# Kernel tuning notes

Hardware: AMD Instinct MI355X
Metric: run time of the kernel (lower is better)

The kernel has to match this reference:

```python
import jax, jax.numpy as jnp
import numpy as np
from jax import lax

LOW_T = 25.0    # int(0.1 * 255)
HIGH_T = 76.0   # int(0.3 * 255)
HYST_ITERS = 64 # cap on hysteresis propagation sweeps
TG22 = 0.4142135623730951  # tan(22.5 deg)
TG67 = 2.414213562373095   # tan(67.5 deg)

SOBEL_X = jnp.array([[-1., 0., 1.], [-2., 0., 2.], [-1., 0., 1.]], dtype=jnp.float32)
SOBEL_Y = jnp.array([[-1., -2., -1.], [0., 0., 0.], [1., 2., 1.]], dtype=jnp.float32)


def _conv3(x, k):
    # x: [B,H,W]; reflect-101 border like cv2.Sobel default
    xp = jnp.pad(x, ((0, 0), (1, 1), (1, 1)), mode='reflect')
    return lax.conv_general_dilated(xp[:, None], k[None, None], (1, 1), 'VALID')[:, 0]


def _dilate3x3(m):
    # 3x3 max-pool (8-connected dilation); m is nonnegative float 0/1
    return lax.reduce_window(m, jnp.float32(0.0), lax.max, (1, 3, 3), (1, 1, 1), 'SAME')


def canny_edge(image, low, high):
    """Batched Canny. image: [B,C,H,W] in [0,1] -> edges [B,1,H,W] in {0,1}."""
    image = lax.stop_gradient(image)  # mirrors .cpu().detach().numpy()
    B, C, H, W = image.shape
    if C == 3:
        gray = 0.299 * image[:, 0] + 0.587 * image[:, 1] + 0.114 * image[:, 2]
    else:
        gray = image[:, 0]
    # (img*255).astype(np.uint8) == floor toward zero for values in [0,1]
    g = jnp.clip(jnp.floor(gray * 255.0), 0.0, 255.0)

    gx = _conv3(g, SOBEL_X)
    gy = _conv3(g, SOBEL_Y)
    mag = jnp.abs(gx) + jnp.abs(gy)  # cv2 default L2gradient=False -> L1 magnitude

    # --- non-maximum suppression (OpenCV-style direction quantization) ---
    mp = jnp.pad(mag, ((0, 0), (1, 1), (1, 1)))

    def sh(dy, dx):
        return mp[:, 1 + dy:1 + dy + H, 1 + dx:1 + dx + W]

    ax, ay = jnp.abs(gx), jnp.abs(gy)
    horiz = ay <= TG22 * ax              # gradient ~horizontal: compare L/R
    vert = ay >= TG67 * ax               # gradient ~vertical: compare U/D
    diag = ~(horiz | vert)
    same_sign = (gx * gy) >= 0
    d1 = diag & same_sign                # 45 deg diagonal

    keep_h = (mag > sh(0, -1)) & (mag >= sh(0, 1))
    keep_v = (mag > sh(-1, 0)) & (mag >= sh(1, 0))
    keep_d1 = (mag > sh(-1, -1)) & (mag >= sh(1, 1))
    keep_d2 = (mag > sh(-1, 1)) & (mag >= sh(1, -1))
    keep = jnp.where(horiz, keep_h,
           jnp.where(vert, keep_v,
           jnp.where(d1, keep_d1, keep_d2)))
    nms = jnp.where(keep, mag, 0.0)

    # --- double threshold + hysteresis (iterative 8-connected propagation) ---
    weak = (nms > low).astype(jnp.float32)
    strong = (nms > high).astype(jnp.float32)

    def cond(state):
        cur, prev, i = state
        return jnp.logical_and(i < HYST_ITERS, jnp.any(cur != prev))

    def body(state):
        cur, prev, i = state
        new = jnp.minimum(_dilate3x3(cur), weak)          # grow strong into weak
        new = jnp.maximum(new, strong)
        return new, cur, i + 1

    edges, _, _ = lax.while_loop(cond, body, (strong, -jnp.ones_like(strong), 0))
    return edges[:, None]  # [B,1,H,W]


def reference(image_A, image_B):
    image_A = jnp.where(image_A.max() > 1, image_A / 2.0, image_A)
    image_B = jnp.where(image_B.max() > 1, image_B / 2.0, image_B)
    edges_A = canny_edge(image_A, LOW_T, HIGH_T)
    edges_B = canny_edge(image_B, LOW_T, HIGH_T)
    diff = edges_A - edges_B
    return jnp.sqrt(jnp.sum(diff * diff))  # Frobenius norm over all elements


def setup_inputs() -> dict:
    key = jax.random.key(0)
    kA, kB = jax.random.split(key)
    image_A = jax.random.uniform(kA, (32, 3, 512, 512), dtype=jnp.float32)
    image_B = jax.random.uniform(kB, (32, 3, 512, 512), dtype=jnp.float32)
    return {"image_A": image_A, "image_B": image_B}
```

## Files before the change

### kernel.cpp

```cpp
#include <hip/hip_runtime.h>
#include <cstdint>

#define IMG_H 512
#define IMG_W 512
#define WPR 8

typedef unsigned long long u64;

__global__ __launch_bounds__(256) void canny_nms_kernel(
    const float* __restrict__ imgA, const float* __restrict__ imgB,
    u64* __restrict__ strong_out, u64* __restrict__ weak_out)
{
    const int img = blockIdx.z;
    const int ty0 = blockIdx.y * 64;
    const int tx0 = blockIdx.x * 64;
    const float* src = (img < 32) ? imgA + (size_t)img * 3 * IMG_H * IMG_W
                                  : imgB + (size_t)(img - 32) * 3 * IMG_H * IMG_W;

    __shared__ float sg[68][68];
    __shared__ float smag[66][66];
    const int tid = threadIdx.x;

    for (int idx = tid; idx < 68 * 68; idx += 256) {
        int ly = idx / 68, lx = idx - ly * 68;
        int iy = ty0 - 2 + ly, ix = tx0 - 2 + lx;
        iy = iy < 0 ? -iy : (iy > IMG_H - 1 ? 2 * (IMG_H - 1) - iy : iy);
        ix = ix < 0 ? -ix : (ix > IMG_W - 1 ? 2 * (IMG_W - 1) - ix : ix);
        size_t p = (size_t)iy * IMG_W + ix;
        float r   = src[p];
        float gch = src[(size_t)IMG_H * IMG_W + p];
        float b   = src[(size_t)2 * IMG_H * IMG_W + p];
        float gray = 0.299f * r + 0.587f * gch + 0.114f * b;
        sg[ly][lx] = fminf(fmaxf(floorf(gray * 255.0f), 0.0f), 255.0f);
    }
    __syncthreads();

    for (int idx = tid; idx < 66 * 66; idx += 256) {
        int ly = idx / 66, lx = idx - ly * 66;
        int iy = ty0 - 1 + ly, ix = tx0 - 1 + lx;
        float m = 0.0f;
        if (iy >= 0 && iy < IMG_H && ix >= 0 && ix < IMG_W) {
            int a = ly + 1, b = lx + 1;
            float tl = sg[a-1][b-1], tc = sg[a-1][b], tr = sg[a-1][b+1];
            float ml = sg[a][b-1],                    mr = sg[a][b+1];
            float bl = sg[a+1][b-1], bc = sg[a+1][b], br = sg[a+1][b+1];
            float gx = (tr + 2.0f*mr + br) - (tl + 2.0f*ml + bl);
            float gy = (bl + 2.0f*bc + br) - (tl + 2.0f*tc + tr);
            m = fabsf(gx) + fabsf(gy);
        }
        smag[ly][lx] = m;
    }
    __syncthreads();

    const int lane = tid & 63;
    const int wv = tid >> 6;
    for (int ry = wv; ry < 64; ry += 4) {
        int a = ry + 2, b = lane + 2;
        float tl = sg[a-1][b-1], tc = sg[a-1][b], tr = sg[a-1][b+1];
        float ml = sg[a][b-1],                    mr = sg[a][b+1];
        float bl = sg[a+1][b-1], bc = sg[a+1][b], br = sg[a+1][b+1];
        float gx = (tr + 2.0f*mr + br) - (tl + 2.0f*ml + bl);
        float gy = (bl + 2.0f*bc + br) - (tl + 2.0f*tc + tr);
        float ax = fabsf(gx), ay = fabsf(gy);
        int my = ry + 1, mx = lane + 1;
        float mag  = smag[my][mx];
        float n_l  = smag[my][mx-1],   n_r  = smag[my][mx+1];
        float n_t  = smag[my-1][mx],   n_b  = smag[my+1][mx];
        float n_tl = smag[my-1][mx-1], n_br = smag[my+1][mx+1];
        float n_tr = smag[my-1][mx+1], n_bl = smag[my+1][mx-1];
        bool horiz = ay <= 0.4142135623730951f * ax;
        bool vert  = ay >= 2.414213562373095f * ax;
        bool d1 = (!(horiz || vert)) && (gx * gy >= 0.0f);
        bool keep_h  = (mag > n_l)  && (mag >= n_r);
        bool keep_v  = (mag > n_t)  && (mag >= n_b);
        bool keep_d1 = (mag > n_tl) && (mag >= n_br);
        bool keep_d2 = (mag > n_tr) && (mag >= n_bl);
        bool keep = horiz ? keep_h : (vert ? keep_v : (d1 ? keep_d1 : keep_d2));
        float nms = keep ? mag : 0.0f;
        u64 wweak   = __ballot(nms > 25.0f);
        u64 wstrong = __ballot(nms > 76.0f);
        if (lane == 0) {
            size_t o = ((size_t)img * IMG_H + (ty0 + ry)) * WPR + blockIdx.x;
            weak_out[o]   = wweak;
            strong_out[o] = wstrong;
        }
    }
}

__global__ __launch_bounds__(256) void hyst_kernel(
    const u64* __restrict__ strong_in, const u64* __restrict__ weak_in,
    u64* __restrict__ edges)
{
    const int img = blockIdx.z;
    const int ty = blockIdx.y, tx = blockIdx.x;
    const int t = threadIdx.x;

    __shared__ u64 sh[4][256];
    __shared__ int sflag;

    const int row0 = ty * 128 - 64;
    const int wc0  = tx * 2 - 1;
    const size_t ibase = (size_t)img * IMG_H * WPR;

    u64 c[4], wk[4];
    {
        int gr = row0 + t;
        bool rok = (gr >= 0 && gr < IMG_H);
        #pragma unroll
        for (int j = 0; j < 4; ++j) {
            int wc = wc0 + j;
            bool ok = rok && wc >= 0 && wc < WPR;
            size_t o = ibase + (size_t)gr * WPR + wc;
            c[j]  = ok ? strong_in[o] : 0ULL;
            wk[j] = ok ? weak_in[o]   : 0ULL;
        }
    }
    if (t == 0) sflag = 0;
    __syncthreads();

    for (int it = 0; it < 64; ++it) {
        u64 h[4];
        h[0] = c[0] | (c[0] << 1) | (c[0] >> 1) | (c[1] << 63);
        h[1] = c[1] | (c[1] << 1) | (c[1] >> 1) | (c[0] >> 63) | (c[2] << 63);
        h[2] = c[2] | (c[2] << 1) | (c[2] >> 1) | (c[1] >> 63) | (c[3] << 63);
        h[3] = c[3] | (c[3] << 1) | (c[3] >> 1) | (c[2] >> 63);
        #pragma unroll
        for (int j = 0; j < 4; ++j) sh[j][t] = h[j];
        __syncthreads();

        u64 n[4] = {h[0], h[1], h[2], h[3]};
        if (t > 0) {
            #pragma unroll
            for (int j = 0; j < 4; ++j) n[j] |= sh[j][t - 1];
        }
        if (t < 255) {
            #pragma unroll
            for (int j = 0; j < 4; ++j) n[j] |= sh[j][t + 1];
        }
        #pragma unroll
        for (int j = 0; j < 4; ++j) n[j] &= wk[j];

        u64 delta = (n[0] ^ c[0]) | (n[1] ^ c[1]) | (n[2] ^ c[2]) | (n[3] ^ c[3]);
        if (delta) sflag = 1;
        __syncthreads();
        int f = sflag;
        __syncthreads();
        if (t == 0) sflag = 0;
        #pragma unroll
        for (int j = 0; j < 4; ++j) c[j] = n[j];
        if (!f) break;
    }

    if (t >= 64 && t < 192) {
        int gr = row0 + t;
        size_t o = ibase + (size_t)gr * WPR;
        edges[o + (wc0 + 1)] = c[1];
        edges[o + (wc0 + 2)] = c[2];
    }
}

__global__ __launch_bounds__(256) void diff_kernel(
    const u64* __restrict__ edges, unsigned int* __restrict__ counter)
{
    size_t i = (size_t)blockIdx.x * 256 + threadIdx.x;
    size_t p = i >> 12;
    size_t k = i & 4095;
    u64 a = edges[p * 4096 + k];
    u64 b = edges[(p + 32) * 4096 + k];
    unsigned int v = (unsigned int)__popcll(a ^ b);
    #pragma unroll
    for (int off = 32; off > 0; off >>= 1) v += __shfl_down(v, off);
    if ((threadIdx.x & 63) == 0) atomicAdd(counter, v);
}

__global__ void finalize_kernel(const unsigned int* __restrict__ counter,
                                float* __restrict__ out)
{
    out[0] = sqrtf((float)(*counter));
}

extern "C" void kernel_launch(void* const* d_in, const int* in_sizes, int n_in,
                              void* d_out, int out_size, void* d_ws, size_t ws_size,
                              hipStream_t stream) {
    const float* imgA = (const float*)d_in[0];
    const float* imgB = (const float*)d_in[1];
    float* out = (float*)d_out;
    char* ws = (char*)d_ws;
    u64* strong_m = (u64*)(ws);
    u64* weak_m   = (u64*)(ws + (2u << 20));
    u64* edges    = (u64*)(ws + (4u << 20));
    unsigned int* counter = (unsigned int*)(ws + (6u << 20));

    hipMemsetAsync(counter, 0, sizeof(unsigned int), stream);

    dim3 g1(8, 8, 64);
    canny_nms_kernel<<<g1, 256, 0, stream>>>(imgA, imgB, strong_m, weak_m);

    dim3 g2(4, 4, 64);
    hyst_kernel<<<g2, 256, 0, stream>>>(strong_m, weak_m, edges);

    diff_kernel<<<512, 256, 0, stream>>>(edges, counter);
    finalize_kernel<<<1, 1, 0, stream>>>(counter, out);
}
```

Baseline: 284.2 us.

## Pack NMS inputs in LDS and fuse hysteresis with diff and finalize

The NMS kernel now stores the gray tile as fp16 and packs an integer magnitude and a quantized direction into one 16-bit LDS word, so the Sobel gradients are no longer recomputed in the NMS pass and LDS traffic shrinks. The hysteresis kernel processes an A/B image pair in one 512-thread block. It computes the XOR popcount directly from shared memory and finalizes the sqrt with a last-block ticket, which removes the edges buffer round trip and two launches. The convergence check drops one barrier by using an iteration-tagged flag, but both images in a pair now iterate until the slower one converges.

```diff
diff --git a/kernel.cpp b/kernel.cpp
--- a/kernel.cpp
+++ b/kernel.cpp
@@ -17,8 +17,8 @@
     const float* src = (img < 32) ? imgA + (size_t)img * 3 * IMG_H * IMG_W
                                   : imgB + (size_t)(img - 32) * 3 * IMG_H * IMG_W;
 
-    __shared__ float sg[68][68];
-    __shared__ float smag[66][66];
+    __shared__ _Float16 sg[68][68];
+    __shared__ unsigned short su[66][66];
     const int tid = threadIdx.x;
 
     for (int idx = tid; idx < 68 * 68; idx += 256) {
@@ -31,54 +31,49 @@
         float gch = src[(size_t)IMG_H * IMG_W + p];
         float b   = src[(size_t)2 * IMG_H * IMG_W + p];
         float gray = 0.299f * r + 0.587f * gch + 0.114f * b;
-        sg[ly][lx] = fminf(fmaxf(floorf(gray * 255.0f), 0.0f), 255.0f);
+        sg[ly][lx] = (_Float16)fminf(fmaxf(floorf(gray * 255.0f), 0.0f), 255.0f);
     }
     __syncthreads();
 
     for (int idx = tid; idx < 66 * 66; idx += 256) {
         int ly = idx / 66, lx = idx - ly * 66;
         int iy = ty0 - 1 + ly, ix = tx0 - 1 + lx;
-        float m = 0.0f;
-        if (iy >= 0 && iy < IMG_H && ix >= 0 && ix < IMG_W) {
+        unsigned short pack = 0;
+        if ((unsigned)iy < (unsigned)IMG_H && (unsigned)ix < (unsigned)IMG_W) {
             int a = ly + 1, b = lx + 1;
-            float tl = sg[a-1][b-1], tc = sg[a-1][b], tr = sg[a-1][b+1];
-            float ml = sg[a][b-1],                    mr = sg[a][b+1];
-            float bl = sg[a+1][b-1], bc = sg[a+1][b], br = sg[a+1][b+1];
+            float tl = (float)sg[a-1][b-1], tc = (float)sg[a-1][b], tr = (float)sg[a-1][b+1];
+            float ml = (float)sg[a][b-1],                           mr = (float)sg[a][b+1];
+            float bl = (float)sg[a+1][b-1], bc = (float)sg[a+1][b], br = (float)sg[a+1][b+1];
             float gx = (tr + 2.0f*mr + br) - (tl + 2.0f*ml + bl);
             float gy = (bl + 2.0f*bc + br) - (tl + 2.0f*tc + tr);
-            m = fabsf(gx) + fabsf(gy);
+            float ax = fabsf(gx), ay = fabsf(gy);
+            int mag = (int)(ax + ay);
+            bool horiz = ay <= 0.4142135623730951f * ax;
+            bool vert  = ay >= 2.414213562373095f * ax;
+            int dir = horiz ? 0 : (vert ? 1 : ((gx * gy >= 0.0f) ? 2 : 3));
+            pack = (unsigned short)(mag | (dir << 12));
         }
-        smag[ly][lx] = m;
+        su[ly][lx] = pack;
     }
     __syncthreads();
 
     const int lane = tid & 63;
     const int wv = tid >> 6;
     for (int ry = wv; ry < 64; ry += 4) {
-        int a = ry + 2, b = lane + 2;
-        float tl = sg[a-1][b-1], tc = sg[a-1][b], tr = sg[a-1][b+1];
-        float ml = sg[a][b-1],                    mr = sg[a][b+1];
-        float bl = sg[a+1][b-1], bc = sg[a+1][b], br = sg[a+1][b+1];
-        float gx = (tr + 2.0f*mr + br) - (tl + 2.0f*ml + bl);
-        float gy = (bl + 2.0f*bc + br) - (tl + 2.0f*tc + tr);
-        float ax = fabsf(gx), ay = fabsf(gy);
         int my = ry + 1, mx = lane + 1;
-        float mag  = smag[my][mx];
-        float n_l  = smag[my][mx-1],   n_r  = smag[my][mx+1];
-        float n_t  = smag[my-1][mx],   n_b  = smag[my+1][mx];
-        float n_tl = smag[my-1][mx-1], n_br = smag[my+1][mx+1];
-        float n_tr = smag[my-1][mx+1], n_bl = smag[my+1][mx-1];
-        bool horiz = ay <= 0.4142135623730951f * ax;
-        bool vert  = ay >= 2.414213562373095f * ax;
-        bool d1 = (!(horiz || vert)) && (gx * gy >= 0.0f);
-        bool keep_h  = (mag > n_l)  && (mag >= n_r);
-        bool keep_v  = (mag > n_t)  && (mag >= n_b);
-        bool keep_d1 = (mag > n_tl) && (mag >= n_br);
-        bool keep_d2 = (mag > n_tr) && (mag >= n_bl);
-        bool keep = horiz ? keep_h : (vert ? keep_v : (d1 ? keep_d1 : keep_d2));
-        float nms = keep ? mag : 0.0f;
-        u64 wweak   = __ballot(nms > 25.0f);
-        u64 wstrong = __ballot(nms > 76.0f);
+        int vc   = su[my][mx];
+        int magc = vc & 0xFFF, dir = vc >> 12;
+        int n_l  = su[my][mx-1]   & 0xFFF, n_r  = su[my][mx+1]   & 0xFFF;
+        int n_t  = su[my-1][mx]   & 0xFFF, n_b  = su[my+1][mx]   & 0xFFF;
+        int n_tl = su[my-1][mx-1] & 0xFFF, n_br = su[my+1][mx+1] & 0xFFF;
+        int n_tr = su[my-1][mx+1] & 0xFFF, n_bl = su[my+1][mx-1] & 0xFFF;
+        bool keep = (dir == 0) ? (magc > n_l  && magc >= n_r)
+                  : (dir == 1) ? (magc > n_t  && magc >= n_b)
+                  : (dir == 2) ? (magc > n_tl && magc >= n_br)
+                               : (magc > n_tr && magc >= n_bl);
+        int nms = keep ? magc : 0;
+        u64 wweak   = __ballot(nms > 25);
+        u64 wstrong = __ballot(nms > 76);
         if (lane == 0) {
             size_t o = ((size_t)img * IMG_H + (ty0 + ry)) * WPR + blockIdx.x;
             weak_out[o]   = wweak;
@@ -87,15 +82,18 @@
     }
 }
 
-__global__ __launch_bounds__(256) void hyst_kernel(
+__global__ __launch_bounds__(512) void hyst_diff_kernel(
     const u64* __restrict__ strong_in, const u64* __restrict__ weak_in,
-    u64* __restrict__ edges)
+    unsigned int* __restrict__ sum, unsigned int* __restrict__ done,
+    float* __restrict__ out)
 {
-    const int img = blockIdx.z;
+    const int pair = blockIdx.z;
     const int ty = blockIdx.y, tx = blockIdx.x;
-    const int t = threadIdx.x;
+    const int half = threadIdx.x >> 8;
+    const int t = threadIdx.x & 255;
+    const int img = pair + (half ? 32 : 0);
 
-    __shared__ u64 sh[4][256];
+    __shared__ u64 sh[2][4][256];
     __shared__ int sflag;
 
     const int row0 = ty * 128 - 64;
@@ -115,8 +113,7 @@
             wk[j] = ok ? weak_in[o]   : 0ULL;
         }
     }
-    if (t == 0) sflag = 0;
-    __syncthreads();
+    if (threadIdx.x == 0) sflag = 0;
 
     for (int it = 0; it < 64; ++it) {
         u64 h[4];
@@ -125,58 +122,52 @@
         h[2] = c[2] | (c[2] << 1) | (c[2] >> 1) | (c[1] >> 63) | (c[3] << 63);
         h[3] = c[3] | (c[3] << 1) | (c[3] >> 1) | (c[2] >> 63);
         #pragma unroll
-        for (int j = 0; j < 4; ++j) sh[j][t] = h[j];
+        for (int j = 0; j < 4; ++j) sh[half][j][t] = h[j];
         __syncthreads();
 
         u64 n[4] = {h[0], h[1], h[2], h[3]};
         if (t > 0) {
             #pragma unroll
-            for (int j = 0; j < 4; ++j) n[j] |= sh[j][t - 1];
+            for (int j = 0; j < 4; ++j) n[j] |= sh[half][j][t - 1];
         }
         if (t < 255) {
             #pragma unroll
-            for (int j = 0; j < 4; ++j) n[j] |= sh[j][t + 1];
+            for (int j = 0; j < 4; ++j) n[j] |= sh[half][j][t + 1];
         }
         #pragma unroll
         for (int j = 0; j < 4; ++j) n[j] &= wk[j];
 
         u64 delta = (n[0] ^ c[0]) | (n[1] ^ c[1]) | (n[2] ^ c[2]) | (n[3] ^ c[3]);
-        if (delta) sflag = 1;
+        if (delta) sflag = it + 1;
         __syncthreads();
-        int f = sflag;
-        __syncthreads();
-        if (t == 0) sflag = 0;
         #pragma unroll
         for (int j = 0; j < 4; ++j) c[j] = n[j];
-        if (!f) break;
+        if (sflag != it + 1) break;
     }
 
-    if (t >= 64 && t < 192) {
-        int gr = row0 + t;
-        size_t o = ibase + (size_t)gr * WPR;
-        edges[o + (wc0 + 1)] = c[1];
-        edges[o + (wc0 + 2)] = c[2];
+    sh[half][0][t] = c[1];
+    sh[half][1][t] = c[2];
+    __syncthreads();
+
+    unsigned int v = 0;
+    if (half == 0 && t >= 64 && t < 192) {
+        v  = (unsigned int)__popcll(sh[0][0][t] ^ sh[1][0][t]);
+        v += (unsigned int)__popcll(sh[0][1][t] ^ sh[1][1][t]);
     }
-}
-
-__global__ __launch_bounds__(256) void diff_kernel(
-    const u64* __restrict__ edges, unsigned int* __restrict__ counter)
-{
-    size_t i = (size_t)blockIdx.x * 256 + threadIdx.x;
-    size_t p = i >> 12;
-    size_t k = i & 4095;
-    u64 a = edges[p * 4096 + k];
-    u64 b = edges[(p + 32) * 4096 + k];
-    unsigned int v = (unsigned int)__popcll(a ^ b);
     #pragma unroll
     for (int off = 32; off > 0; off >>= 1) v += __shfl_down(v, off);
-    if ((threadIdx.x & 63) == 0) atomicAdd(counter, v);
-}
+    if ((threadIdx.x & 63) == 0 && v != 0) atomicAdd(sum, v);
+    __syncthreads();
 
-__global__ void finalize_kernel(const unsigned int* __restrict__ counter,
-                                float* __restrict__ out)
-{
-    out[0] = sqrtf((float)(*counter));
+    if (threadIdx.x == 0) {
+        __threadfence();
+        unsigned int ticket = atomicAdd(done, 1);
+        if (ticket == 4 * 4 * 32 - 1) {
+            __threadfence();
+            unsigned int s = atomicAdd(sum, 0u);
+            out[0] = sqrtf((float)s);
+        }
+    }
 }
 
 extern "C" void kernel_launch(void* const* d_in, const int* in_sizes, int n_in,
@@ -188,17 +179,14 @@
     char* ws = (char*)d_ws;
     u64* strong_m = (u64*)(ws);
     u64* weak_m   = (u64*)(ws + (2u << 20));
-    u64* edges    = (u64*)(ws + (4u << 20));
-    unsigned int* counter = (unsigned int*)(ws + (6u << 20));
+    unsigned int* counters = (unsigned int*)(ws + (4u << 20));
 
-    hipMemsetAsync(counter, 0, sizeof(unsigned int), stream);
+    hipMemsetAsync(counters, 0, 2 * sizeof(unsigned int), stream);
 
     dim3 g1(8, 8, 64);
     canny_nms_kernel<<<g1, 256, 0, stream>>>(imgA, imgB, strong_m, weak_m);
 
-    dim3 g2(4, 4, 64);
-    hyst_kernel<<<g2, 256, 0, stream>>>(strong_m, weak_m, edges);
-
-    diff_kernel<<<512, 256, 0, stream>>>(edges, counter);
-    finalize_kernel<<<1, 1, 0, stream>>>(counter, out);
+    dim3 g2(4, 4, 32);
+    hyst_diff_kernel<<<g2, 512, 0, stream>>>(strong_m, weak_m,
+                                             counters, counters + 1, out);
 }
```

Result: no change. 282.5 us (-0.6%).
